# Kernel tuning notes

Measured on AMD Instinct MI355X. Metric: run time of the kernel, lower is better.

The kernel has to match this reference:

```python
import jax, jax.numpy as jnp
import numpy as np

N_NODES = 50000
N_EDGES = 800000
D = 128            # in_channels == hidden_channels
N_LAYERS = 3
OUT = 16
N_GRAPHS = 128


def setup_inputs() -> dict:
    key = jax.random.key(0)
    ks = jax.random.split(key, 12)
    x = jax.random.normal(ks[0], (N_NODES, D), dtype=jnp.float32)
    edge_index = jax.random.randint(ks[1], (2, N_EDGES), 0, N_NODES, dtype=jnp.int64)
    batch_ids = jnp.sort(jax.random.randint(ks[2], (N_NODES,), 0, N_GRAPHS, dtype=jnp.int64))
    s = 1.0 / np.sqrt(D)
    # Stacked per-layer GraphConv weights (all layers are D->D here).
    Wrel = jax.random.uniform(ks[3], (N_LAYERS, D, D), jnp.float32, -s, s)
    brel = jax.random.uniform(ks[4], (N_LAYERS, D), jnp.float32, -s, s)
    Wroot = jax.random.uniform(ks[5], (N_LAYERS, D, D), jnp.float32, -s, s)
    # post_mp MLP head
    W1 = jax.random.uniform(ks[6], (D, D), jnp.float32, -s, s)
    b1 = jax.random.uniform(ks[7], (D,), jnp.float32, -s, s)
    W2 = jax.random.uniform(ks[8], (D, OUT), jnp.float32, -s, s)
    b2 = jax.random.uniform(ks[9], (OUT,), jnp.float32, -s, s)
    return {"x": x, "edge_index": edge_index, "batch_ids": batch_ids,
            "Wrel": Wrel, "brel": brel, "Wroot": Wroot,
            "W1": W1, "b1": b1, "W2": W2, "b2": b2}


def reference(x, edge_index, batch_ids, Wrel, brel, Wroot, W1, b1, W2, b2):
    src, dst = edge_index[0], edge_index[1]
    h = x
    for l in range(N_LAYERS):
        # GraphConv: lin_rel(sum_{j->i} h_j) + lin_root(h_i)
        agg = jax.ops.segment_sum(h[src], dst, num_segments=N_NODES)  # [N, D]
        h = agg @ Wrel[l] + brel[l] + h @ Wroot[l]
        h = jax.nn.relu(h)
        # dropout p=0.0 / eval mode -> identity
    # global mean pool over graphs
    sums = jax.ops.segment_sum(h, batch_ids, num_segments=N_GRAPHS)          # [G, D]
    counts = jax.ops.segment_sum(jnp.ones((N_NODES,), h.dtype), batch_ids,
                                 num_segments=N_GRAPHS)                       # [G]
    pooled = sums / jnp.maximum(counts, 1.0)[:, None]
    # post_mp MLP (dropout identity in eval)
    out = (pooled @ W1 + b1) @ W2 + b2                                        # [G, OUT]
    return out
```

## Files before the change

### kernel.cpp

```cpp
#include <hip/hip_runtime.h>

#define N_NODES 50000
#define N_EDGES 800000
#define D 128
#define N_LAYERS 3
#define OUT_F 16
#define N_GRAPHS 128
#define NBUCK 391
#define EPB 4096
#define NB3 ((N_EDGES + EPB - 1) / EPB)
#define CAP 4096
#define NT32 ((N_NODES + 31) / 32)
#define NGB ((NT32 + 7) / 8)
#define PITCH 132
#define NCAST 6250
#define NPREPW 96

typedef __attribute__((ext_vector_type(8))) short short8;
typedef __attribute__((ext_vector_type(16))) float floatx16;

__device__ __forceinline__ unsigned short f2bf(float f) {
  unsigned int u = __float_as_uint(f);
  u += 0x7fff + ((u >> 16) & 1);
  return (unsigned short)(u >> 16);
}
__device__ __forceinline__ float bf2f(unsigned short b) {
  return __uint_as_float(((unsigned int)b) << 16);
}
__device__ __forceinline__ float blo(unsigned v) { return __uint_as_float(v << 16); }
__device__ __forceinline__ float bhi(unsigned v) { return __uint_as_float(v & 0xffff0000u); }

__global__ __launch_bounds__(256) void partition_kernel(
    const int* __restrict__ src, const int* __restrict__ dst,
    int* __restrict__ cursor, unsigned* __restrict__ pairs) {
  __shared__ unsigned pk[EPB];
  __shared__ int hist[NBUCK];
  __shared__ int wcur[NBUCK];
  const int e0 = blockIdx.x * EPB;
  const int n = min(EPB, N_EDGES - e0);
  const int t = threadIdx.x;
  for (int i = t; i < NBUCK; i += 256) hist[i] = 0;
  __syncthreads();
  for (int i = t; i < n; i += 256) {
    int d = dst[e0 + i], s = src[e0 + i];
    pk[i] = ((unsigned)d << 16) | (unsigned)s;
    atomicAdd(&hist[d >> 7], 1);
  }
  __syncthreads();
  for (int i = t; i < NBUCK; i += 256)
    wcur[i] = i * CAP + (hist[i] ? atomicAdd(&cursor[i], hist[i]) : 0);
  __syncthreads();
  for (int i = t; i < n; i += 256) {
    unsigned p = pk[i];
    int pos = atomicAdd(&wcur[p >> 23], 1);
    pairs[pos] = p;
  }
}

__global__ __launch_bounds__(256) void bucket_sort_kernel(
    const unsigned* __restrict__ pairs, const int* __restrict__ cursor,
    int* __restrict__ rowbeg, int* __restrict__ rowend, int* __restrict__ esrc) {
  __shared__ unsigned pk[CAP];
  __shared__ int sorted[CAP];
  __shared__ int hist[128], off[128], cur[128];
  const int bkt = blockIdx.x;
  const int t = threadIdx.x;
  const int beg = bkt * CAP;
  const int cnt = cursor[bkt];
  if (t < 128) hist[t] = 0;
  __syncthreads();
  for (int i = t; i < cnt; i += 256) {
    unsigned p = pairs[beg + i];
    pk[i] = p;
    atomicAdd(&hist[(p >> 16) & 127], 1);
  }
  __syncthreads();
  if (t < 128) off[t] = hist[t];
  __syncthreads();
  for (int o = 1; o < 128; o <<= 1) {
    int x = (t < 128 && t >= o) ? off[t - o] : 0;
    __syncthreads();
    if (t < 128) off[t] += x;
    __syncthreads();
  }
  if (t < 128) {
    int node = bkt * 128 + t;
    if (node < N_NODES) {
      rowbeg[node] = beg + off[t] - hist[t];
      rowend[node] = beg + off[t];
    }
    cur[t] = off[t] - hist[t];
  }
  __syncthreads();
  for (int i = t; i < cnt; i += 256) {
    unsigned p = pk[i];
    int pos = atomicAdd(&cur[(p >> 16) & 127], 1);
    sorted[pos] = (int)(p & 0xFFFFu);
  }
  __syncthreads();
  for (int i = t; i < cnt; i += 256) esrc[beg + i] = sorted[i];
}

__global__ __launch_bounds__(256) void prep_all_kernel(
    const float* __restrict__ x, unsigned short* __restrict__ x16,
    const float* __restrict__ Wrel, const float* __restrict__ Wroot,
    unsigned short* __restrict__ wt, int* __restrict__ cursor) {
  const int bid = blockIdx.x;
  const int t = threadIdx.x;
  if (bid < NCAST) {
    const int i = bid * 256 + t;
    const float4 v = *(const float4*)&x[(size_t)i * 4];
    uint2 o;
    o.x = f2bf(v.x) | ((unsigned)f2bf(v.y) << 16);
    o.y = f2bf(v.z) | ((unsigned)f2bf(v.w) << 16);
    *(uint2*)&x16[(size_t)i * 4] = o;
  } else if (bid < NCAST + NPREPW) {
    const int idx = (bid - NCAST) * 256 + t;
    const int lane = idx & 63;
    const int kst = (idx >> 6) & 31;
    const int nt = (idx >> 11) & 1;
    const int half = (idx >> 12) & 1;
    const int l = idx >> 13;
    const int n = half * 64 + nt * 32 + (lane & 31);
    const int kx0 = kst * 16 + (lane >> 5) * 8;
    const int seg = kx0 >> 7;
    const int k0 = kx0 & 127;
    const int mat = seg >> 1, lo = seg & 1;
    const float* W = (mat ? Wroot : Wrel) + (size_t)l * D * D;
    unsigned short v[8];
#pragma unroll
    for (int j = 0; j < 8; ++j) {
      float w = W[(size_t)(k0 + j) * D + n];
      unsigned short hi = f2bf(w);
      v[j] = lo ? f2bf(w - bf2f(hi)) : hi;
    }
    unsigned short* dstp =
        wt + ((size_t)l * 128 + (half * 2 + nt) * 32 + kst) * 512 + lane * 8;
    *(uint4*)dstp = *(const uint4*)v;
  } else {
    const int i = (bid - NCAST - NPREPW) * 256 + t;
    if (i < NBUCK) cursor[i] = 0;
  }
}

__global__ __launch_bounds__(256) void agg_kernel(
    const unsigned short* __restrict__ h,
    const int* __restrict__ rowbeg, const int* __restrict__ rowend,
    const int* __restrict__ esrc, unsigned short* __restrict__ agg) {
  const int idx = blockIdx.x * 256 + threadIdx.x;
  const int n = idx >> 4;
  const int lane = idx & 15;
  if (n >= N_NODES) return;
  const int beg = rowbeg[n], end = rowend[n];
  float a0 = 0, a1 = 0, a2 = 0, a3 = 0, a4 = 0, a5 = 0, a6 = 0, a7 = 0;
  int e = beg;
  for (; e + 4 <= end; e += 4) {
    const int s0 = esrc[e],     s1 = esrc[e + 1];
    const int s2 = esrc[e + 2], s3 = esrc[e + 3];
    const uint4 v0 = *(const uint4*)&h[(size_t)s0 * D + lane * 8];
    const uint4 v1 = *(const uint4*)&h[(size_t)s1 * D + lane * 8];
    const uint4 v2 = *(const uint4*)&h[(size_t)s2 * D + lane * 8];
    const uint4 v3 = *(const uint4*)&h[(size_t)s3 * D + lane * 8];
    a0 += blo(v0.x) + blo(v1.x) + blo(v2.x) + blo(v3.x);
    a1 += bhi(v0.x) + bhi(v1.x) + bhi(v2.x) + bhi(v3.x);
    a2 += blo(v0.y) + blo(v1.y) + blo(v2.y) + blo(v3.y);
    a3 += bhi(v0.y) + bhi(v1.y) + bhi(v2.y) + bhi(v3.y);
    a4 += blo(v0.z) + blo(v1.z) + blo(v2.z) + blo(v3.z);
    a5 += bhi(v0.z) + bhi(v1.z) + bhi(v2.z) + bhi(v3.z);
    a6 += blo(v0.w) + blo(v1.w) + blo(v2.w) + blo(v3.w);
    a7 += bhi(v0.w) + bhi(v1.w) + bhi(v2.w) + bhi(v3.w);
  }
  for (; e < end; ++e) {
    const int s0 = esrc[e];
    const uint4 v0 = *(const uint4*)&h[(size_t)s0 * D + lane * 8];
    a0 += blo(v0.x); a1 += bhi(v0.x);
    a2 += blo(v0.y); a3 += bhi(v0.y);
    a4 += blo(v0.z); a5 += bhi(v0.z);
    a6 += blo(v0.w); a7 += bhi(v0.w);
  }
  uint4 o;
  o.x = f2bf(a0) | ((unsigned)f2bf(a1) << 16);
  o.y = f2bf(a2) | ((unsigned)f2bf(a3) << 16);
  o.z = f2bf(a4) | ((unsigned)f2bf(a5) << 16);
  o.w = f2bf(a6) | ((unsigned)f2bf(a7) << 16);
  *(uint4*)&agg[(size_t)n * D + lane * 8] = o;
}

__global__ __launch_bounds__(512, 2) void gemm_kernel(
    const unsigned short* __restrict__ agg, const unsigned short* __restrict__ hv,
    const unsigned short* __restrict__ wt,
    const float* __restrict__ brel,
    unsigned short* __restrict__ outp) {
  __shared__ unsigned short lds[32768];
  const int t = threadIdx.x;
  const int wave = t >> 6, lane = t & 63;
  const int g = t >> 4, li = t & 15;
  const int r2 = lane & 31, hseg = lane >> 5;
  const int tile = blockIdx.x * 8 + wave;

  short8 ag[8], hh[8];
#pragma unroll
  for (int r = 0; r < 4; ++r) {
#pragma unroll
    for (int j = 0; j < 4; ++j) {
      int srow = (blockIdx.x * 8 + 2 * r + (j >> 1)) * 32 + g;
      if (srow >= N_NODES) srow = N_NODES - 1;
      const unsigned short* sp = (j & 1) ? hv : agg;
      *(uint4*)&lds[(j * 32 + g) * PITCH + li * 8] =
          *(const uint4*)&sp[(size_t)srow * D + li * 8];
    }
    __syncthreads();
    if ((wave >> 1) == r) {
      const int slot = wave & 1;
#pragma unroll
      for (int i = 0; i < 8; ++i) {
        ag[i] = *(const short8*)&lds[(slot * 2 + 0) * 32 * PITCH +
                                     r2 * PITCH + i * 16 + hseg * 8];
        hh[i] = *(const short8*)&lds[(slot * 2 + 1) * 32 * PITCH +
                                     r2 * PITCH + i * 16 + hseg * 8];
      }
    }
    __syncthreads();
  }

  const int r0 = tile * 32;
#pragma unroll
  for (int pp = 0; pp < 2; ++pp) {
    const unsigned short* ws = wt + (size_t)pp * 32768;
#pragma unroll
    for (int j = 0; j < 8; ++j) {
      const int idx = t + j * 512;
      *(uint4*)&lds[idx * 8] = *(const uint4*)&ws[idx * 8];
    }
    __syncthreads();
#pragma unroll
    for (int p2 = 0; p2 < 2; ++p2) {
      floatx16 acc = {0.f};
#pragma unroll
      for (int kst = 0; kst < 32; ++kst) {
        const short8 af = (kst < 16) ? ag[kst & 7] : hh[kst & 7];
        const short8 b = *(const short8*)&lds[(p2 * 32 + kst) * 512 + lane * 8];
        acc = __builtin_amdgcn_mfma_f32_32x32x16_bf16(af, b, acc, 0, 0, 0);
      }
      const int cb = (pp * 2 + p2) * 32 + r2;
      const float bias = brel[cb];
#pragma unroll
      for (int reg = 0; reg < 16; ++reg) {
        const int orow = r0 + (reg & 3) + 8 * (reg >> 2) + 4 * hseg;
        if (orow < N_NODES)
          outp[(size_t)orow * D + cb] = f2bf(fmaxf(acc[reg] + bias, 0.f));
      }
    }
    __syncthreads();
  }
}

__device__ __forceinline__ int lb_search(const int* __restrict__ a, int n, int key) {
  int lo = 0, hi = n;
  while (lo < hi) {
    int m = (lo + hi) >> 1;
    if (a[m] < key) lo = m + 1; else hi = m;
  }
  return lo;
}

__global__ __launch_bounds__(256) void pool_head_kernel(
    const unsigned short* __restrict__ h, const int* __restrict__ batch,
    const float* __restrict__ W1, const float* __restrict__ b1,
    const float* __restrict__ W2, const float* __restrict__ b2,
    float* __restrict__ out) {
  __shared__ float sums_lds[16][128];
  __shared__ float pooled[128];
  __shared__ float hidden[128];
  __shared__ int range[2];
  const int g = blockIdx.x;
  const int t = threadIdx.x;
  if (t < 2) range[t] = lb_search(batch, N_NODES, g + t);
  __syncthreads();
  const int lo = range[0], hi = range[1];
  const int rg = t >> 4, cg = t & 15;
  float a0 = 0, a1 = 0, a2 = 0, a3 = 0, a4 = 0, a5 = 0, a6 = 0, a7 = 0;
  for (int n = lo + rg; n < hi; n += 16) {
    const uint4 v = *(const uint4*)&h[(size_t)n * D + cg * 8];
    a0 += blo(v.x); a1 += bhi(v.x);
    a2 += blo(v.y); a3 += bhi(v.y);
    a4 += blo(v.z); a5 += bhi(v.z);
    a6 += blo(v.w); a7 += bhi(v.w);
  }
  sums_lds[rg][cg * 8 + 0] = a0; sums_lds[rg][cg * 8 + 1] = a1;
  sums_lds[rg][cg * 8 + 2] = a2; sums_lds[rg][cg * 8 + 3] = a3;
  sums_lds[rg][cg * 8 + 4] = a4; sums_lds[rg][cg * 8 + 5] = a5;
  sums_lds[rg][cg * 8 + 6] = a6; sums_lds[rg][cg * 8 + 7] = a7;
  __syncthreads();
  if (t < 128) {
    float s = 0.f;
#pragma unroll
    for (int r = 0; r < 16; ++r) s += sums_lds[r][t];
    pooled[t] = s / fmaxf((float)(hi - lo), 1.f);
  }
  __syncthreads();
  if (t < 128) {
    float a = b1[t];
    for (int k = 0; k < D; ++k) a += pooled[k] * W1[k * D + t];
    hidden[t] = a;
  }
  __syncthreads();
  if (t < OUT_F) {
    float o = b2[t];
    for (int k = 0; k < D; ++k) o += hidden[k] * W2[k * OUT_F + t];
    out[(size_t)g * OUT_F + t] = o;
  }
}

extern "C" void kernel_launch(void* const* d_in, const int* in_sizes, int n_in,
                              void* d_out, int out_size, void* d_ws, size_t ws_size,
                              hipStream_t stream) {
  const float* x     = (const float*)d_in[0];
  const int*   ei    = (const int*)d_in[1];
  const int*   batch = (const int*)d_in[2];
  const float* Wrel  = (const float*)d_in[3];
  const float* brel  = (const float*)d_in[4];
  const float* Wroot = (const float*)d_in[5];
  const float* W1    = (const float*)d_in[6];
  const float* b1    = (const float*)d_in[7];
  const float* W2    = (const float*)d_in[8];
  const float* b2    = (const float*)d_in[9];
  float* out = (float*)d_out;

  const size_t ND = (size_t)N_NODES * D;
  unsigned short* bufA = (unsigned short*)d_ws;
  unsigned short* bufB = bufA + ND;
  unsigned short* bufC = bufB + ND;
  unsigned short* wt   = bufC + ND;
  int* rowbeg = (int*)(wt + (size_t)N_LAYERS * 128 * 512);
  int* rowend = rowbeg + N_NODES;
  int* esrc   = rowend + N_NODES;
  unsigned* pairs = (unsigned*)(esrc + (size_t)NBUCK * CAP);
  int* cursor = (int*)(pairs + (size_t)NBUCK * CAP);

  const int* esrc_in = ei;
  const int* edst_in = ei + N_EDGES;

  prep_all_kernel<<<NCAST + NPREPW + 2, 256, 0, stream>>>(
      x, bufC, Wrel, Wroot, wt, cursor);
  partition_kernel<<<NB3, 256, 0, stream>>>(esrc_in, edst_in, cursor, pairs);
  bucket_sort_kernel<<<NBUCK, 256, 0, stream>>>(pairs, cursor, rowbeg, rowend, esrc);

  const size_t WL = (size_t)128 * 512;
  const int agg_blocks = (N_NODES * 16 + 255) / 256;
  agg_kernel<<<agg_blocks, 256, 0, stream>>>(bufC, rowbeg, rowend, esrc, bufB);
  gemm_kernel<<<NGB, 512, 0, stream>>>(bufB, bufC, wt, brel, bufA);
  agg_kernel<<<agg_blocks, 256, 0, stream>>>(bufA, rowbeg, rowend, esrc, bufB);
  gemm_kernel<<<NGB, 512, 0, stream>>>(bufB, bufA, wt + WL, brel + D, bufC);
  agg_kernel<<<agg_blocks, 256, 0, stream>>>(bufC, rowbeg, rowend, esrc, bufB);
  gemm_kernel<<<NGB, 512, 0, stream>>>(bufB, bufC, wt + 2 * WL, brel + 2 * D, bufA);

  pool_head_kernel<<<N_GRAPHS, 256, 0, stream>>>(bufA, batch, W1, b1, W2, b2, out);
}
```

Baseline: 277.3 us.

## Load GEMM A operands directly from global and halve GEMM block size

The GEMM kernel no longer stages the aggregated and root activation rows through LDS in four synchronized rounds. Each wave now loads its own 32-row A fragments straight from global memory into registers. Blocks shrink from 8 waves to 4, which doubles the grid, and the trailing barrier is moved so the weight LDS buffer is only guarded between the two weight halves. The aim is to cut LDS round-trips and barriers in the prologue. In exchange, each lane issues strided 16-byte global loads that may coalesce less well, and every block reloads the full weight matrix, so weight traffic doubles.

```diff
diff --git a/kernel.cpp b/kernel.cpp
--- a/kernel.cpp
+++ b/kernel.cpp
@@ -11,8 +11,7 @@
 #define NB3 ((N_EDGES + EPB - 1) / EPB)
 #define CAP 4096
 #define NT32 ((N_NODES + 31) / 32)
-#define NGB ((NT32 + 7) / 8)
-#define PITCH 132
+#define NGB4 ((NT32 + 3) / 4)
 #define NCAST 6250
 #define NPREPW 96
 
@@ -186,60 +185,46 @@
   *(uint4*)&agg[(size_t)n * D + lane * 8] = o;
 }
 
-__global__ __launch_bounds__(512, 2) void gemm_kernel(
+__global__ __launch_bounds__(256, 2) void gemm_kernel(
     const unsigned short* __restrict__ agg, const unsigned short* __restrict__ hv,
     const unsigned short* __restrict__ wt,
     const float* __restrict__ brel,
     unsigned short* __restrict__ outp) {
-  __shared__ unsigned short lds[32768];
+  __shared__ unsigned short blds[32768];
   const int t = threadIdx.x;
   const int wave = t >> 6, lane = t & 63;
-  const int g = t >> 4, li = t & 15;
   const int r2 = lane & 31, hseg = lane >> 5;
-  const int tile = blockIdx.x * 8 + wave;
+  const int tile = blockIdx.x * 4 + wave;
+  const int r0 = tile * 32;
+  int arow = r0 + r2;
+  if (arow >= N_NODES) arow = N_NODES - 1;
 
   short8 ag[8], hh[8];
-#pragma unroll
-  for (int r = 0; r < 4; ++r) {
-#pragma unroll
-    for (int j = 0; j < 4; ++j) {
-      int srow = (blockIdx.x * 8 + 2 * r + (j >> 1)) * 32 + g;
-      if (srow >= N_NODES) srow = N_NODES - 1;
-      const unsigned short* sp = (j & 1) ? hv : agg;
-      *(uint4*)&lds[(j * 32 + g) * PITCH + li * 8] =
-          *(const uint4*)&sp[(size_t)srow * D + li * 8];
+  const unsigned short* ap = agg + (size_t)arow * D + hseg * 8;
+  const unsigned short* hp = hv + (size_t)arow * D + hseg * 8;
+#pragma unroll
+  for (int i = 0; i < 8; ++i) {
+    ag[i] = *(const short8*)(ap + i * 16);
+    hh[i] = *(const short8*)(hp + i * 16);
+  }
+
+#pragma unroll
+  for (int pp = 0; pp < 2; ++pp) {
+    if (pp) __syncthreads();
+    const unsigned short* ws = wt + (size_t)pp * 32768;
+#pragma unroll
+    for (int j = 0; j < 16; ++j) {
+      const int idx = t + j * 256;
+      *(uint4*)&blds[idx * 8] = *(const uint4*)&ws[idx * 8];
     }
     __syncthreads();
-    if ((wave >> 1) == r) {
-      const int slot = wave & 1;
-#pragma unroll
-      for (int i = 0; i < 8; ++i) {
-        ag[i] = *(const short8*)&lds[(slot * 2 + 0) * 32 * PITCH +
-                                     r2 * PITCH + i * 16 + hseg * 8];
-        hh[i] = *(const short8*)&lds[(slot * 2 + 1) * 32 * PITCH +
-                                     r2 * PITCH + i * 16 + hseg * 8];
-      }
-    }
-    __syncthreads();
-  }
-
-  const int r0 = tile * 32;
-#pragma unroll
-  for (int pp = 0; pp < 2; ++pp) {
-    const unsigned short* ws = wt + (size_t)pp * 32768;
-#pragma unroll
-    for (int j = 0; j < 8; ++j) {
-      const int idx = t + j * 512;
-      *(uint4*)&lds[idx * 8] = *(const uint4*)&ws[idx * 8];
-    }
-    __syncthreads();
 #pragma unroll
     for (int p2 = 0; p2 < 2; ++p2) {
       floatx16 acc = {0.f};
 #pragma unroll
       for (int kst = 0; kst < 32; ++kst) {
         const short8 af = (kst < 16) ? ag[kst & 7] : hh[kst & 7];
-        const short8 b = *(const short8*)&lds[(p2 * 32 + kst) * 512 + lane * 8];
+        const short8 b = *(const short8*)&blds[(p2 * 32 + kst) * 512 + lane * 8];
         acc = __builtin_amdgcn_mfma_f32_32x32x16_bf16(af, b, acc, 0, 0, 0);
       }
       const int cb = (pp * 2 + p2) * 32 + r2;
@@ -251,7 +236,6 @@
           outp[(size_t)orow * D + cb] = f2bf(fmaxf(acc[reg] + bias, 0.f));
       }
     }
-    __syncthreads();
   }
 }
 
@@ -349,11 +333,11 @@
   const size_t WL = (size_t)128 * 512;
   const int agg_blocks = (N_NODES * 16 + 255) / 256;
   agg_kernel<<<agg_blocks, 256, 0, stream>>>(bufC, rowbeg, rowend, esrc, bufB);
-  gemm_kernel<<<NGB, 512, 0, stream>>>(bufB, bufC, wt, brel, bufA);
+  gemm_kernel<<<NGB4, 256, 0, stream>>>(bufB, bufC, wt, brel, bufA);
   agg_kernel<<<agg_blocks, 256, 0, stream>>>(bufA, rowbeg, rowend, esrc, bufB);
-  gemm_kernel<<<NGB, 512, 0, stream>>>(bufB, bufA, wt + WL, brel + D, bufC);
+  gemm_kernel<<<NGB4, 256, 0, stream>>>(bufB, bufA, wt + WL, brel + D, bufC);
   agg_kernel<<<agg_blocks, 256, 0, stream>>>(bufC, rowbeg, rowend, esrc, bufB);
-  gemm_kernel<<<NGB, 512, 0, stream>>>(bufB, bufC, wt + 2 * WL, brel + 2 * D, bufA);
+  gemm_kernel<<<NGB4, 256, 0, stream>>>(bufB, bufC, wt + 2 * WL, brel + 2 * D, bufA);
 
   pool_head_kernel<<<N_GRAPHS, 256, 0, stream>>>(bufA, batch, W1, b1, W2, b2, out);
 }
```

After: 274.1 us. Within noise of the previous version (-1.1%).
